# Performance work log

Hardware: AMD Instinct MI355X
Metric: run time of the kernel (lower is better)

## Reference

```python
import jax, jax.numpy as jnp
import numpy as np

K = 2          # kernel_size
STRIDE = 1
C_IN = 2       # n_channels (hardcoded in module)
NQ = K * K     # 4 qubits
PI = np.pi


def _apply_1q(state, gate, wire):
    # state: [N, 16] complex64; gate: [N,2,2] (batched) or [2,2] (shared)
    N = state.shape[0]
    s = state.reshape((N,) + (2,) * NQ)
    s = jnp.moveaxis(s, 1 + wire, NQ)          # wire axis -> last
    s = s.reshape(N, -1, 2)
    if gate.ndim == 3:
        s = jnp.einsum('nab,nkb->nka', gate, s)
    else:
        s = jnp.einsum('ab,nkb->nka', gate, s)
    s = s.reshape((N,) + (2,) * NQ)
    s = jnp.moveaxis(s, NQ, 1 + wire)
    return s.reshape(N, -1)


def _apply_cnot(state, ctrl, tgt):
    N = state.shape[0]
    s = state.reshape((N,) + (2,) * NQ)
    s = jnp.moveaxis(s, (1 + ctrl, 1 + tgt), (NQ - 1, NQ))
    shp = s.shape
    s = s.reshape(N, -1, 2, 2)                 # [..., ctrl, tgt]
    s = jnp.concatenate([s[:, :, :1, :], s[:, :, 1:, ::-1]], axis=2)
    s = s.reshape(shp)
    s = jnp.moveaxis(s, (NQ - 1, NQ), (1 + ctrl, 1 + tgt))
    return s.reshape(N, -1)


def _rx(theta):
    # theta: [N] or scalar -> [N,2,2] or [2,2] complex
    c = jnp.cos(theta / 2).astype(jnp.complex64)
    s = (-1j) * jnp.sin(theta / 2).astype(jnp.complex64)
    return jnp.stack([jnp.stack([c, s], -1), jnp.stack([s, c], -1)], -2)


def _ry(theta):
    c = jnp.cos(theta / 2)
    s = jnp.sin(theta / 2)
    return jnp.stack([jnp.stack([c, -s], -1), jnp.stack([s, c], -1)], -2).astype(jnp.complex64)


def _circuit(angles, weights):
    # angles: [N, 8]; weights: [L, 4]. Returns expval(PauliZ) per wire: [N, 4].
    N = angles.shape[0]
    state = jnp.zeros((N, 2 ** NQ), jnp.complex64).at[:, 0].set(1.0)
    for i in range(NQ):
        state = _apply_1q(state, _rx(angles[:, 2 * i]), i)
        state = _apply_1q(state, _ry(angles[:, 2 * i + 1]), i)
    # BasicEntanglerLayers: per layer RX(w[l,i]) on wire i, then CNOT ring
    for l in range(weights.shape[0]):
        for i in range(NQ):
            state = _apply_1q(state, _rx(weights[l, i]), i)
        for i in range(NQ):
            state = _apply_cnot(state, i, (i + 1) % NQ)
    p = state.real ** 2 + state.imag ** 2
    p = p.reshape((N,) + (2,) * NQ)
    ez = [jnp.sum(jnp.take(p, 0, axis=1 + w) - jnp.take(p, 1, axis=1 + w),
                  axis=tuple(range(1, NQ))) for w in range(NQ)]
    return jnp.stack(ez, -1)


def _forward(x, weights):
    B, C, H, W = x.shape
    nh = (H - K) // STRIDE + 1
    nw = (W - K) // STRIDE + 1
    # unfold: [B, C, nh, nw, K*K] with patch-element order (kh, kw)
    subs = [x[:, :, kh:kh + (nh - 1) * STRIDE + 1:STRIDE,
                    kw:kw + (nw - 1) * STRIDE + 1:STRIDE]
            for kh in range(K) for kw in range(K)]
    patches = jnp.stack(subs, axis=-1)                      # [B,C,nh,nw,KK]
    patches = patches.transpose(0, 2, 3, 4, 1)              # [B,nh,nw,KK,C]
    patches = patches.reshape(B, nh * nw, K * K * C)
    # per-sample min-max normalize to [0, pi]
    flat = patches.reshape(B, -1)
    pmin = flat.min(axis=1)[:, None, None]
    pmax = flat.max(axis=1)[:, None, None]
    angles = (patches - pmin) / (pmax - pmin + 1e-8) * PI
    angles = angles.reshape(B * nh * nw, K * K * C)
    out = _circuit(angles, weights)                         # [B*nh*nw, 4]
    return out.reshape(B, nh, nw, NQ).transpose(0, 3, 1, 2)


def setup_inputs() -> dict:
    key = jax.random.key(0)
    k1, k2 = jax.random.split(key)
    x = jax.random.normal(k1, (8, C_IN, 224, 224), dtype=jnp.float32)
    weights = jax.random.uniform(k2, (1, NQ), dtype=jnp.float32) * (2 * PI)
    return {"x": x, "weights": weights}


def reference(x, weights):
    return _forward(x, weights)
```

## Files before the change

kernel.cpp:

```cpp
#include <hip/hip_runtime.h>
#include <math.h>

#define BATCH 8
#define CIN   2
#define H     224
#define W     224
#define NH    223
#define NW    223
#define PIXB  (H * W)
#define NPB   (CIN * H * W)
#define PER_B (NH * NW)
#define BPB   32
#define TPR   56
#define SLOTS (NH * TPR)
#define QBLK  ((SLOTS + 255) / 256)
#define PI_F  3.14159265358979323846f


__global__ __launch_bounds__(256) void minmax_kernel(
        const float* __restrict__ x, const float* __restrict__ wts,
        float* __restrict__ ws) {
    if (blockIdx.x == 0 && threadIdx.x < 4) {
        float s, c;
        __sincosf(wts[threadIdx.x], &s, &c);
        ws[512 + threadIdx.x] = s;
        ws[516 + threadIdx.x] = c;
    }
    int b  = blockIdx.x / BPB;
    int cb = blockIdx.x % BPB;
    const float4* xb = (const float4*)(x + (size_t)b * NPB);
    const int per = (NPB / 4) / BPB;
    float lmin =  INFINITY, lmax = -INFINITY;
    for (int idx = cb * per + threadIdx.x; idx < (cb + 1) * per; idx += 256) {
        float4 v = xb[idx];
        lmin = fminf(lmin, fminf(fminf(v.x, v.y), fminf(v.z, v.w)));
        lmax = fmaxf(lmax, fmaxf(fmaxf(v.x, v.y), fmaxf(v.z, v.w)));
    }
    #pragma unroll
    for (int off = 32; off > 0; off >>= 1) {
        lmin = fminf(lmin, __shfl_down(lmin, off, 64));
        lmax = fmaxf(lmax, __shfl_down(lmax, off, 64));
    }
    __shared__ float smin[4], smax[4];
    int wid = threadIdx.x >> 6;
    if ((threadIdx.x & 63) == 0) { smin[wid] = lmin; smax[wid] = lmax; }
    __syncthreads();
    if (threadIdx.x == 0) {
        #pragma unroll
        for (int i = 1; i < 4; ++i) {
            lmin = fminf(lmin, smin[i]);
            lmax = fmaxf(lmax, smax[i]);
        }
        ws[b * BPB + cb]       = lmin;
        ws[256 + b * BPB + cb] = lmax;
    }
}

__global__ __launch_bounds__(256) void quanv_kernel(
        const float* __restrict__ x, const float* __restrict__ ws,
        float* __restrict__ out) {
    const int b = blockIdx.y;
    __shared__ float sred[2];
    if (threadIdx.x < 32) {
        float mn = ws[b * BPB + threadIdx.x];
        float mx = ws[256 + b * BPB + threadIdx.x];
        #pragma unroll
        for (int off = 16; off > 0; off >>= 1) {
            mn = fminf(mn, __shfl_xor(mn, off, 32));
            mx = fmaxf(mx, __shfl_xor(mx, off, 32));
        }
        if (threadIdx.x == 0) { sred[0] = mn; sred[1] = mx; }
    }
    __syncthreads();
    const float gmin  = sred[0];
    const float scale = PI_F / (sred[1] - gmin + 1e-8f);

    const float sw0 = ws[512], sw1 = ws[513], sw2 = ws[514], sw3 = ws[515];
    const float cw0 = ws[516], cw1 = ws[517], cw2 = ws[518], cw3 = ws[519];

    int slot = blockIdx.x * 256 + threadIdx.x;
    if (slot >= SLOTS) return;
    int i  = slot / TPR;
    int jt = (slot - i * TPR) * 4;
    const int npos = (jt == 220) ? 3 : 4;

    const float* r0 = x + (size_t)b * NPB + i * W + jt;
    const float* r1 = r0 + W;
    const float* r2 = r0 + PIXB;
    const float* r3 = r2 + W;
    float4 v0 = *(const float4*)r0;
    float4 v1 = *(const float4*)r1;
    float4 v2 = *(const float4*)r2;
    float4 v3 = *(const float4*)r3;
    float e0 = 0.f, e1 = 0.f, e2 = 0.f, e3 = 0.f;
    if (jt < 220) { e0 = r0[4]; e1 = r1[4]; e2 = r2[4]; e3 = r3[4]; }

    const float p0[5] = {v0.x, v0.y, v0.z, v0.w, e0};
    const float p1[5] = {v1.x, v1.y, v1.z, v1.w, e1};
    const float p2[5] = {v2.x, v2.y, v2.z, v2.w, e2};
    const float p3[5] = {v3.x, v3.y, v3.z, v3.w, e3};

    float sa0[5], ca0[5], sa1[5], ca1[5], cb0[5], cb1[5];
    #pragma unroll
    for (int k = 0; k < 5; ++k) {
        __sincosf((p0[k] - gmin) * scale, &sa0[k], &ca0[k]);
        __sincosf((p1[k] - gmin) * scale, &sa1[k], &ca1[k]);
        cb0[k] = __cosf((p2[k] - gmin) * scale);
        cb1[k] = __cosf((p3[k] - gmin) * scale);
    }

    const size_t obase = (size_t)b * 4 * PER_B + (size_t)i * NW + jt;
    #pragma unroll
    for (int p = 0; p < 4; ++p) {
        if (p < npos) {
            float z0 = ca0[p]     * cb0[p]     * cw0 - sa0[p]     * sw0;
            float z1 = ca0[p + 1] * cb0[p + 1] * cw1 - sa0[p + 1] * sw1;
            float z2 = ca1[p]     * cb1[p]     * cw2 - sa1[p]     * sw2;
            float z3 = ca1[p + 1] * cb1[p + 1] * cw3 - sa1[p + 1] * sw3;
            float z01 = z0 * z1;
            out[obase + p]             = z1 * z2 * z3;
            out[obase + PER_B + p]     = z01;
            out[obase + 2 * PER_B + p] = z01 * z2;
            out[obase + 3 * PER_B + p] = z01 * z2 * z3;
        }
    }
}

extern "C" void kernel_launch(void* const* d_in, const int* in_sizes, int n_in,
                              void* d_out, int out_size, void* d_ws, size_t ws_size,
                              hipStream_t stream) {
    const float* x   = (const float*)d_in[0];
    const float* wts = (const float*)d_in[1];
    float* out = (float*)d_out;
    float* ws  = (float*)d_ws;

    minmax_kernel<<<BATCH * BPB, 256, 0, stream>>>(x, wts, ws);
    quanv_kernel<<<dim3(QBLK, BATCH), 256, 0, stream>>>(x, ws, out);
}
```

Before: 62.51 us.

## Fuse min-max reduction into quanv kernel with per-block redundant reduction

```diff
diff --git a/kernel.cpp b/kernel.cpp
--- a/kernel.cpp
+++ b/kernel.cpp
@@ -9,29 +9,21 @@
 #define NW    223
 #define PIXB  (H * W)
 #define NPB   (CIN * H * W)
+#define N4    (NPB / 4)
 #define PER_B (NH * NW)
-#define BPB   32
 #define TPR   56
 #define SLOTS (NH * TPR)
 #define QBLK  ((SLOTS + 255) / 256)
 #define PI_F  3.14159265358979323846f
 
+__global__ __launch_bounds__(256) void fused_quanv(
+        const float* __restrict__ x, const float* __restrict__ wts,
+        float* __restrict__ out) {
+    const int b = blockIdx.y;
 
-__global__ __launch_bounds__(256) void minmax_kernel(
-        const float* __restrict__ x, const float* __restrict__ wts,
-        float* __restrict__ ws) {
-    if (blockIdx.x == 0 && threadIdx.x < 4) {
-        float s, c;
-        __sincosf(wts[threadIdx.x], &s, &c);
-        ws[512 + threadIdx.x] = s;
-        ws[516 + threadIdx.x] = c;
-    }
-    int b  = blockIdx.x / BPB;
-    int cb = blockIdx.x % BPB;
     const float4* xb = (const float4*)(x + (size_t)b * NPB);
-    const int per = (NPB / 4) / BPB;
     float lmin =  INFINITY, lmax = -INFINITY;
-    for (int idx = cb * per + threadIdx.x; idx < (cb + 1) * per; idx += 256) {
+    for (int idx = threadIdx.x; idx < N4; idx += 256) {
         float4 v = xb[idx];
         lmin = fminf(lmin, fminf(fminf(v.x, v.y), fminf(v.z, v.w)));
         lmax = fmaxf(lmax, fmaxf(fmaxf(v.x, v.y), fmaxf(v.z, v.w)));
@@ -41,8 +33,8 @@
         lmin = fminf(lmin, __shfl_down(lmin, off, 64));
         lmax = fmaxf(lmax, __shfl_down(lmax, off, 64));
     }
-    __shared__ float smin[4], smax[4];
-    int wid = threadIdx.x >> 6;
+    __shared__ float smin[4], smax[4], sred[2];
+    const int wid = threadIdx.x >> 6;
     if ((threadIdx.x & 63) == 0) { smin[wid] = lmin; smax[wid] = lmax; }
     __syncthreads();
     if (threadIdx.x == 0) {
@@ -51,37 +43,21 @@
             lmin = fminf(lmin, smin[i]);
             lmax = fmaxf(lmax, smax[i]);
         }
-        ws[b * BPB + cb]       = lmin;
-        ws[256 + b * BPB + cb] = lmax;
-    }
-}
-
-__global__ __launch_bounds__(256) void quanv_kernel(
-        const float* __restrict__ x, const float* __restrict__ ws,
-        float* __restrict__ out) {
-    const int b = blockIdx.y;
-    __shared__ float sred[2];
-    if (threadIdx.x < 32) {
-        float mn = ws[b * BPB + threadIdx.x];
-        float mx = ws[256 + b * BPB + threadIdx.x];
-        #pragma unroll
-        for (int off = 16; off > 0; off >>= 1) {
-            mn = fminf(mn, __shfl_xor(mn, off, 32));
-            mx = fmaxf(mx, __shfl_xor(mx, off, 32));
-        }
-        if (threadIdx.x == 0) { sred[0] = mn; sred[1] = mx; }
+        sred[0] = lmin;
+        sred[1] = lmax;
     }
     __syncthreads();
     const float gmin  = sred[0];
     const float scale = PI_F / (sred[1] - gmin + 1e-8f);
 
-    const float sw0 = ws[512], sw1 = ws[513], sw2 = ws[514], sw3 = ws[515];
-    const float cw0 = ws[516], cw1 = ws[517], cw2 = ws[518], cw3 = ws[519];
+    float sw[4], cw[4];
+    #pragma unroll
+    for (int q = 0; q < 4; ++q) __sincosf(wts[q], &sw[q], &cw[q]);
 
-    int slot = blockIdx.x * 256 + threadIdx.x;
+    const int slot = blockIdx.x * 256 + threadIdx.x;
     if (slot >= SLOTS) return;
-    int i  = slot / TPR;
-    int jt = (slot - i * TPR) * 4;
+    const int i  = slot / TPR;
+    const int jt = (slot - i * TPR) * 4;
     const int npos = (jt == 220) ? 3 : 4;
 
     const float* r0 = x + (size_t)b * NPB + i * W + jt;
@@ -113,10 +89,10 @@
     #pragma unroll
     for (int p = 0; p < 4; ++p) {
         if (p < npos) {
-            float z0 = ca0[p]     * cb0[p]     * cw0 - sa0[p]     * sw0;
-            float z1 = ca0[p + 1] * cb0[p + 1] * cw1 - sa0[p + 1] * sw1;
-            float z2 = ca1[p]     * cb1[p]     * cw2 - sa1[p]     * sw2;
-            float z3 = ca1[p + 1] * cb1[p + 1] * cw3 - sa1[p + 1] * sw3;
+            float z0 = ca0[p]     * cb0[p]     * cw[0] - sa0[p]     * sw[0];
+            float z1 = ca0[p + 1] * cb0[p + 1] * cw[1] - sa0[p + 1] * sw[1];
+            float z2 = ca1[p]     * cb1[p]     * cw[2] - sa1[p]     * sw[2];
+            float z3 = ca1[p + 1] * cb1[p + 1] * cw[3] - sa1[p + 1] * sw[3];
             float z01 = z0 * z1;
             out[obase + p]             = z1 * z2 * z3;
             out[obase + PER_B + p]     = z01;
@@ -132,8 +108,6 @@
     const float* x   = (const float*)d_in[0];
     const float* wts = (const float*)d_in[1];
     float* out = (float*)d_out;
-    float* ws  = (float*)d_ws;
 
-    minmax_kernel<<<BATCH * BPB, 256, 0, stream>>>(x, wts, ws);
-    quanv_kernel<<<dim3(QBLK, BATCH), 256, 0, stream>>>(x, ws, out);
+    fused_quanv<<<dim3(QBLK, BATCH), 256, 0, stream>>>(x, wts, out);
 }
```

New measurement: 84.83 us. 1.36x slower.
